# Kernel optimization log

Hardware: AMD Instinct MI355X
Metric: run time of the kernel (lower is better)

Reference implementation:

```python
import jax, jax.numpy as jnp
import numpy as np

B, N, NEV, E, D, L = 4, 20000, 100000, 400000, 64, 3

def setup_inputs() -> dict:
    key = jax.random.key(0)
    ks = jax.random.split(key, 12)
    x = jax.random.normal(ks[0], (B, N, 3), dtype=jnp.float32)
    # channel 0 is the susceptible boolean mask (0/1)
    mask0 = (jax.random.uniform(ks[1], (B, N)) < 0.3).astype(jnp.float32)
    x = x.at[..., 0].set(mask0)
    dag_edge_index = jax.random.randint(ks[2], (2, E), 0, NEV, dtype=jnp.int64)
    event_to_node = jax.random.randint(ks[3], (NEV,), 0, N, dtype=jnp.int64)
    event_src_node = jax.random.randint(ks[4], (NEV,), 0, N, dtype=jnp.int64)
    s = 1.0 / np.sqrt(D)
    Wp = jax.random.normal(ks[5], (6, D), dtype=jnp.float32) * (1.0 / np.sqrt(6))
    bp = jnp.zeros((D,), dtype=jnp.float32)
    Ws = jax.random.normal(ks[6], (L, D, D), dtype=jnp.float32) * s
    Wa = jax.random.normal(ks[7], (L, D, D), dtype=jnp.float32) * s
    ba = jnp.zeros((L, D), dtype=jnp.float32)
    Wo = jax.random.normal(ks[8], (D,), dtype=jnp.float32) * s
    bo = jnp.zeros((), dtype=jnp.float32)
    return {"x": x, "Wp": Wp, "bp": bp, "Ws": Ws, "Wa": Wa, "ba": ba,
            "Wo": Wo, "bo": bo, "dag_edge_index": dag_edge_index,
            "event_to_node": event_to_node, "event_src_node": event_src_node}

def reference(x, Wp, bp, Ws, Wa, ba, Wo, bo, dag_edge_index, event_to_node, event_src_node):
    n_events = event_src_node.shape[0]
    # event features: [B, n_events, 6] -> project -> ReLU
    ev_feat = jnp.concatenate([x[:, event_src_node, :], x[:, event_to_node, :]], axis=-1)
    h = jax.nn.relu(ev_feat @ Wp + bp)  # [B, n_events, D]
    # reversed DAG edges: src = dag[1], dst = dag[0]
    src_e, dst_e = dag_edge_index[1], dag_edge_index[0]
    deg = jnp.zeros((n_events,), h.dtype).at[dst_e].add(1.0)
    deg = jnp.maximum(deg, 1.0)[None, :, None]
    for l in range(Ws.shape[0]):
        agg = jnp.zeros_like(h).at[:, dst_e].add(h[:, src_e])  # scatter-add mean agg
        h = jax.nn.relu(h @ Ws[l] + (agg / deg) @ Wa[l] + ba[l])
    # aggregate events back to nodes (mean)
    node_emb = jnp.zeros((x.shape[0], x.shape[1], h.shape[-1]), h.dtype).at[:, event_to_node].add(h)
    count = jnp.zeros((x.shape[1],), h.dtype).at[event_to_node].add(1.0)
    node_emb = node_emb / jnp.maximum(count, 1.0)[None, :, None]
    scores = node_emb @ Wo + bo  # [B, N]
    susceptible = x[..., 0] > 0
    scores = jnp.where(susceptible, -jnp.inf, scores)
    return jax.nn.log_softmax(scores, axis=-1)
```

## Files before the change

### kernel.cpp

```cpp
#include <hip/hip_runtime.h>
#include <hip/hip_bf16.h>
#include <math.h>

constexpr int B   = 4;
constexpr int N   = 20000;
constexpr int NEV = 100000;
constexpr int E   = 400000;
constexpr int D   = 64;
constexpr int L   = 3;
constexpr int CAP = 32;
constexpr int CHUNK = 625;
constexpr size_t HBYTES = (size_t)B * NEV * D + 256;

typedef short  short8 __attribute__((ext_vector_type(8)));
typedef float  f32x4  __attribute__((ext_vector_type(4)));
typedef float  f32x2  __attribute__((ext_vector_type(2)));


__device__ inline unsigned short f2bu(float f) {
  union { __hip_bfloat16 b; unsigned short s; } u;
  u.b = __float2bfloat16(f);
  return u.s;
}
__device__ inline unsigned packbf(float lo, float hi) {
  return ((unsigned)f2bu(hi) << 16) | (unsigned)f2bu(lo);
}
__device__ inline void cvt16(float* a, uint4 v) {
  unsigned vv[4] = {v.x, v.y, v.z, v.w};
#pragma unroll
  for (int i = 0; i < 4; ++i) {
    f32x2 lo = __builtin_amdgcn_cvt_pk_f32_fp8((int)vv[i], false);
    f32x2 hi = __builtin_amdgcn_cvt_pk_f32_fp8((int)vv[i], true);
    a[4 * i + 0] = lo[0]; a[4 * i + 1] = lo[1];
    a[4 * i + 2] = hi[0]; a[4 * i + 3] = hi[1];
  }
}
__device__ inline void add16(float* a, uint4 v) {
  unsigned vv[4] = {v.x, v.y, v.z, v.w};
#pragma unroll
  for (int i = 0; i < 4; ++i) {
    f32x2 lo = __builtin_amdgcn_cvt_pk_f32_fp8((int)vv[i], false);
    f32x2 hi = __builtin_amdgcn_cvt_pk_f32_fp8((int)vv[i], true);
    a[4 * i + 0] += lo[0]; a[4 * i + 1] += lo[1];
    a[4 * i + 2] += hi[0]; a[4 * i + 3] += hi[1];
  }
}
__device__ inline short8 pack8(const float* f) {
  union { unsigned u[4]; short8 s; } r;
#pragma unroll
  for (int i = 0; i < 4; ++i) r.u[i] = packbf(f[2 * i], f[2 * i + 1]);
  return r.s;
}
__device__ __forceinline__ void round4(const unsigned char* gb,
                                       const int* cr, int p, float* a) {
  int4 idx = *(const int4*)(cr + p);
  uint4 v0 = *(const uint4*)(gb + (size_t)idx.x * 256);
  uint4 v1 = *(const uint4*)(gb + (size_t)idx.y * 256);
  uint4 v2 = *(const uint4*)(gb + (size_t)idx.z * 256);
  uint4 v3 = *(const uint4*)(gb + (size_t)idx.w * 256);
  add16(a, v0); add16(a, v1); add16(a, v2); add16(a, v3);
}


__global__ void k_zero(float4* __restrict__ p, int n4) {
  int i = blockIdx.x * blockDim.x + threadIdx.x;
  if (i < n4) p[i] = make_float4(0.f, 0.f, 0.f, 0.f);
}

__global__ void k_fill(int4* __restrict__ csrc4,
                       uint4* __restrict__ h0z, uint4* __restrict__ h1z) {
  int i = blockIdx.x * blockDim.x + threadIdx.x;
  if (i < NEV * CAP / 4) csrc4[i] = make_int4(NEV, NEV, NEV, NEV);
  int z = i - NEV * CAP / 4;
  if (z >= 0 && z < 16) h0z[z] = make_uint4(0u, 0u, 0u, 0u);
  if (z >= 16 && z < 32) h1z[z - 16] = make_uint4(0u, 0u, 0u, 0u);
}

__global__ void k_prep(const int* __restrict__ dag,
                       int* __restrict__ cnt,
                       int* __restrict__ csrc,
                       const int* __restrict__ e2n,
                       int* __restrict__ ncount,
                       const float* __restrict__ Ws,
                       const float* __restrict__ Wa,
                       unsigned short* __restrict__ Wt) {
  int bid = blockIdx.x;
  if (bid < 1563) {
    int i = bid * 256 + threadIdx.x;
    if (i < E) {
      int dst = dag[i];
      int src = dag[E + i];
      int pos = atomicAdd(&cnt[dst], 1);
      if (pos < CAP) csrc[dst * CAP + pos] = src;
    }
  } else if (bid < 1954) {
    int i = (bid - 1563) * 256 + threadIdx.x;
    if (i < NEV) atomicAdd(&ncount[e2n[i]], 1);
  } else {
    int i = (bid - 1954) * 256 + threadIdx.x;
    int l  = i >> 13;
    int r  = i & 8191;
    int n  = r >> 7;
    int s2 = r & 127;
    int hf = s2 >> 6, s = s2 & 63;
    int b  = ((s >> 3) & 3) * 16 + (s >> 5) * 8 + (s & 7);
    int c  = (b & 3) * 16 + (b >> 2);
    float v = hf ? Wa[l * 4096 + c * 64 + n]
                 : Ws[l * 4096 + c * 64 + n];
    Wt[l * 8192 + n * 128 + s2] = f2bu(v);
  }
}

__global__ __launch_bounds__(256) void k_proj(const float* __restrict__ x,
                                              const float* __restrict__ Wp,
                                              const float* __restrict__ bp,
                                              const int* __restrict__ esrc,
                                              const int* __restrict__ e2n,
                                              unsigned* __restrict__ h,
                                              float* __restrict__ nscore) {
  int gid = blockIdx.x * blockDim.x + threadIdx.x;
  if (gid < B * N) nscore[gid] = 0.f;
  const int lane = threadIdx.x & 63;
  const int e    = gid >> 6;
  int sn = esrc[e], tn = e2n[e];
  float xval = 0.f;
  if (lane < 24) {
    int bl = lane / 6, rem = lane % 6;
    int node = (rem < 3) ? sn : tn;
    xval = x[(size_t)(bl * N + node) * 3 + (rem < 3 ? rem : rem - 3)];
  }
  const int b = lane >> 4, p = lane & 15;
  float xv[6];
#pragma unroll
  for (int k = 0; k < 6; ++k) xv[k] = __shfl(xval, b * 6 + k, 64);
  float a[4];
#pragma unroll
  for (int t = 0; t < 4; ++t) {
    int d = p + 16 * t;
    float acc = bp[d];
#pragma unroll
    for (int k = 0; k < 6; ++k) acc += xv[k] * Wp[k * 64 + d];
    a[t] = fmaxf(acc, 0.f);
  }
  int w = __builtin_amdgcn_cvt_pk_fp8_f32(a[0], a[1], 0, false);
  w     = __builtin_amdgcn_cvt_pk_fp8_f32(a[2], a[3], w, true);
  h[e * 64 + lane] = (unsigned)w;
}

template <bool LAST>
__global__ __launch_bounds__(256, 4) void k_layer(
    const unsigned short* __restrict__ Wt,
    const float* __restrict__ ba,
    const float* __restrict__ Wo,
    const int* __restrict__ e2n,
    const int* __restrict__ cnt,
    const int* __restrict__ csrc,
    const unsigned char* __restrict__ h_in,
    unsigned char* __restrict__ h_out,
    float* __restrict__ nscore) {
  const int tid  = threadIdx.x;
  const int wv   = tid >> 6, lane = tid & 63;
  const int e0   = blockIdx.x * 32;
  const int r0   = e0 * 4;
  const int m    = lane & 15, q = lane >> 4;
  const int el   = m >> 2;
  const int bb   = m & 3;
  const int eA   = e0 + wv * 4 + el;
  const int eB   = e0 + 16 + wv * 4 + el;

  const int* crA = csrc + (size_t)eA * CAP;
  const int* crB = csrc + (size_t)eB * CAP;
  int4 iA = *(const int4*)crA;
  int4 iB = *(const int4*)crB;
  uint4 vdA = *(const uint4*)(h_in + (size_t)(r0 + wv * 16 + m) * 64 + q * 16);
  uint4 vdB = *(const uint4*)(h_in + (size_t)(r0 + 64 + wv * 16 + m) * 64 + q * 16);
  int cA = cnt[eA];
  int cB = cnt[eB];

  const unsigned char* gb = h_in + bb * 64 + q * 16;
  float aA[16], aB[16];
#pragma unroll
  for (int i = 0; i < 16; ++i) { aA[i] = 0.f; aB[i] = 0.f; }
  {
    uint4 vA0 = *(const uint4*)(gb + (size_t)iA.x * 256);
    uint4 vA1 = *(const uint4*)(gb + (size_t)iA.y * 256);
    uint4 vA2 = *(const uint4*)(gb + (size_t)iA.z * 256);
    uint4 vA3 = *(const uint4*)(gb + (size_t)iA.w * 256);
    uint4 vB0 = *(const uint4*)(gb + (size_t)iB.x * 256);
    uint4 vB1 = *(const uint4*)(gb + (size_t)iB.y * 256);
    uint4 vB2 = *(const uint4*)(gb + (size_t)iB.z * 256);
    uint4 vB3 = *(const uint4*)(gb + (size_t)iB.w * 256);
    add16(aA, vA0); add16(aA, vA1); add16(aA, vA2); add16(aA, vA3);
    add16(aB, vB0); add16(aB, vB1); add16(aB, vB2); add16(aB, vB3);
  }
  int ccA = min(cA, CAP), ccA16 = min(ccA, 16);
  int ccB = min(cB, CAP), ccB16 = min(ccB, 16);
  for (int p = 4; p < ccA16; p += 4) round4(gb, crA, p, aA);
  for (int p = 4; p < ccB16; p += 4) round4(gb, crB, p, aB);
  for (int j = 16; j < ccA; ++j)
    add16(aA, *(const uint4*)(gb + (size_t)crA[j] * 256));
  for (int j = 16; j < ccB; ++j)
    add16(aB, *(const uint4*)(gb + (size_t)crB[j] * 256));
  {
    float invA = 1.f / fmaxf((float)cA, 1.f);
    float invB = 1.f / fmaxf((float)cB, 1.f);
#pragma unroll
    for (int i = 0; i < 16; ++i) { aA[i] *= invA; aB[i] *= invB; }
  }
  short8 agA0 = pack8(aA), agA1 = pack8(aA + 8);
  short8 agB0 = pack8(aB), agB1 = pack8(aB + 8);

  short8 adA0, adA1, adB0, adB1;
  {
    float f[16];
    cvt16(f, vdA); adA0 = pack8(f); adA1 = pack8(f + 8);
    cvt16(f, vdB); adB0 = pack8(f); adB1 = pack8(f + 8);
  }

  f32x4 accA[4], accB[4];
#pragma unroll
  for (int t = 0; t < 4; ++t) {
    float bv = ba[t * 16 + m];
    accA[t] = (f32x4){bv, bv, bv, bv};
    accB[t] = accA[t];
  }
  const unsigned short* wb = Wt + m * 128 + q * 8;
#pragma unroll
  for (int t = 0; t < 4; ++t) {
    short8 b0 = *(const short8*)(wb + t * 2048 + 0);
    short8 b1 = *(const short8*)(wb + t * 2048 + 32);
    short8 b2 = *(const short8*)(wb + t * 2048 + 64);
    short8 b3 = *(const short8*)(wb + t * 2048 + 96);
    accA[t] = __builtin_amdgcn_mfma_f32_16x16x32_bf16(adA0, b0, accA[t], 0, 0, 0);
    accA[t] = __builtin_amdgcn_mfma_f32_16x16x32_bf16(adA1, b1, accA[t], 0, 0, 0);
    accA[t] = __builtin_amdgcn_mfma_f32_16x16x32_bf16(agA0, b2, accA[t], 0, 0, 0);
    accA[t] = __builtin_amdgcn_mfma_f32_16x16x32_bf16(agA1, b3, accA[t], 0, 0, 0);
    accB[t] = __builtin_amdgcn_mfma_f32_16x16x32_bf16(adB0, b0, accB[t], 0, 0, 0);
    accB[t] = __builtin_amdgcn_mfma_f32_16x16x32_bf16(adB1, b1, accB[t], 0, 0, 0);
    accB[t] = __builtin_amdgcn_mfma_f32_16x16x32_bf16(agB0, b2, accB[t], 0, 0, 0);
    accB[t] = __builtin_amdgcn_mfma_f32_16x16x32_bf16(agB1, b3, accB[t], 0, 0, 0);
  }

  if constexpr (!LAST) {
#pragma unroll
    for (int g = 0; g < 2; ++g) {
      const f32x4* ac = g ? accB : accA;
#pragma unroll
      for (int r = 0; r < 4; ++r) {
        int w = __builtin_amdgcn_cvt_pk_fp8_f32(fmaxf(ac[0][r], 0.f),
                                                fmaxf(ac[1][r], 0.f), 0, false);
        w     = __builtin_amdgcn_cvt_pk_fp8_f32(fmaxf(ac[2][r], 0.f),
                                                fmaxf(ac[3][r], 0.f), w, true);
        int grow = r0 + g * 64 + wv * 16 + q * 4 + r;
        ((unsigned*)h_out)[grow * 16 + m] = (unsigned)w;
      }
    }
  } else {
    float w0 = Wo[m], w1 = Wo[16 + m], w2 = Wo[32 + m], w3 = Wo[48 + m];
#pragma unroll
    for (int g = 0; g < 2; ++g) {
      const f32x4* ac = g ? accB : accA;
#pragma unroll
      for (int r = 0; r < 4; ++r) {
        float v = fmaxf(ac[0][r], 0.f) * w0 + fmaxf(ac[1][r], 0.f) * w1
                + fmaxf(ac[2][r], 0.f) * w2 + fmaxf(ac[3][r], 0.f) * w3;
        v += __shfl_xor(v, 1, 64);
        v += __shfl_xor(v, 2, 64);
        v += __shfl_xor(v, 4, 64);
        v += __shfl_xor(v, 8, 64);
        if (m == 0) {
          int grow = r0 + g * 64 + wv * 16 + q * 4 + r;
          int e = grow >> 2, b = grow & 3;
          atomicAdd(&nscore[b * N + e2n[e]], v);
        }
      }
    }
  }
}

__device__ inline float ls_score(const float* nscore, const int* ncount,
                                 const float* x, float bov, int b, int n) {
  return (x[(size_t)(b * N + n) * 3] > 0.f)
             ? -INFINITY
             : nscore[b * N + n] / fmaxf((float)ncount[n], 1.f) + bov;
}

__global__ __launch_bounds__(256) void k_ls1(const float* __restrict__ nscore,
                                             const int* __restrict__ ncount,
                                             const float* __restrict__ x,
                                             const float* __restrict__ bo,
                                             float* __restrict__ pmax,
                                             float* __restrict__ psum,
                                             float* __restrict__ sc) {
  const int b = blockIdx.x >> 5, ch = blockIdx.x & 31;
  const int n0 = ch * CHUNK;
  const int tid = threadIdx.x;
  const float bov = bo[0];
  float s0 = -INFINITY, s1 = -INFINITY, s2 = -INFINITY;
  if (tid < CHUNK) {
    s0 = ls_score(nscore, ncount, x, bov, b, n0 + tid);
    sc[b * N + n0 + tid] = s0;
  }
  if (tid + 256 < CHUNK) {
    s1 = ls_score(nscore, ncount, x, bov, b, n0 + tid + 256);
    sc[b * N + n0 + tid + 256] = s1;
  }
  if (tid + 512 < CHUNK) {
    s2 = ls_score(nscore, ncount, x, bov, b, n0 + tid + 512);
    sc[b * N + n0 + tid + 512] = s2;
  }
  float m = fmaxf(fmaxf(s0, s1), s2);
  __shared__ float red[4];
#pragma unroll
  for (int o = 32; o; o >>= 1) m = fmaxf(m, __shfl_xor(m, o, 64));
  if ((tid & 63) == 0) red[tid >> 6] = m;
  __syncthreads();
  float pm = fmaxf(fmaxf(red[0], red[1]), fmaxf(red[2], red[3]));
  float pm2 = (pm == -INFINITY) ? 0.f : pm;
  float e = expf(s0 - pm2) + expf(s1 - pm2) + expf(s2 - pm2);
#pragma unroll
  for (int o = 32; o; o >>= 1) e += __shfl_xor(e, o, 64);
  __syncthreads();
  if ((tid & 63) == 0) red[tid >> 6] = e;
  __syncthreads();
  if (tid == 0) {
    pmax[blockIdx.x] = pm;
    psum[blockIdx.x] = red[0] + red[1] + red[2] + red[3];
  }
}

__global__ __launch_bounds__(256) void k_ls3(const float* __restrict__ pmax,
                                             const float* __restrict__ psum,
                                             const float* __restrict__ sc,
                                             float* __restrict__ out) {
  const int b = blockIdx.x >> 5, ch = blockIdx.x & 31;
  const int n0 = ch * CHUNK;
  const int tid = threadIdx.x;
  __shared__ float sgm, slse;
  if (tid < 64) {
    float pm = (tid < 32) ? pmax[b * 32 + tid] : -INFINITY;
    float ps = (tid < 32) ? psum[b * 32 + tid] : 0.f;
    float gm = pm;
#pragma unroll
    for (int o = 32; o; o >>= 1) gm = fmaxf(gm, __shfl_xor(gm, o, 64));
    float gm2 = (gm == -INFINITY) ? 0.f : gm;
    float c = (pm == -INFINITY) ? 0.f : ps * expf(pm - gm2);
#pragma unroll
    for (int o = 32; o; o >>= 1) c += __shfl_xor(c, o, 64);
    if (tid == 0) { sgm = gm; slse = logf(c); }
  }
  __syncthreads();
  const float gm = sgm, lse = slse;
  for (int i = tid; i < CHUNK; i += 256) {
    int n = n0 + i;
    out[b * N + n] = fmaxf(sc[b * N + n] - gm - lse, -3.0e38f);
  }
}

extern "C" void kernel_launch(void* const* d_in, const int* in_sizes, int n_in,
                              void* d_out, int out_size, void* d_ws, size_t ws_size,
                              hipStream_t stream) {
  const float* x   = (const float*)d_in[0];
  const float* Wp  = (const float*)d_in[1];
  const float* bp  = (const float*)d_in[2];
  const float* Ws  = (const float*)d_in[3];
  const float* Wa  = (const float*)d_in[4];
  const float* ba  = (const float*)d_in[5];
  const float* Wo  = (const float*)d_in[6];
  const float* bo  = (const float*)d_in[7];
  const int*   dag = (const int*)d_in[8];
  const int*   e2n = (const int*)d_in[9];
  const int*   esr = (const int*)d_in[10];

  int*   ws     = (int*)d_ws;
  int*   cnt    = ws;
  int*   ncount = ws + 100000;
  float* nscore = (float*)(ws + 120000);
  float* pmax   = (float*)(ws + 200000);
  float* psum   = (float*)(ws + 200128);
  int*   csrc   = ws + 200704;
  unsigned short* Wt = (unsigned short*)(ws + 3400704);
  unsigned char* h0 = (unsigned char*)(ws + 3406912);
  unsigned char* h1 = h0 + HBYTES;
  float* sc     = (float*)(h1 + HBYTES);
  float* out    = (float*)d_out;

  k_zero<<<(30000 + 255) / 256, 256, 0, stream>>>((float4*)ws, 30000);
  k_fill<<<(NEV * CAP / 4 + 32 + 255) / 256, 256, 0, stream>>>(
      (int4*)csrc, (uint4*)(h0 + (size_t)NEV * 256), (uint4*)(h1 + (size_t)NEV * 256));
  k_prep<<<2050, 256, 0, stream>>>(dag, cnt, csrc, e2n, ncount, Ws, Wa, Wt);
  k_proj<<<(B * NEV * 16) / 256, 256, 0, stream>>>(x, Wp, bp, esr, e2n,
                                                   (unsigned*)h0, nscore);

  k_layer<false><<<NEV / 32, 256, 0, stream>>>(Wt,         ba,       Wo, e2n,
                                               cnt, csrc, h0, h1, nscore);
  k_layer<false><<<NEV / 32, 256, 0, stream>>>(Wt + 8192,  ba + D,   Wo, e2n,
                                               cnt, csrc, h1, h0, nscore);
  k_layer<true><<<NEV / 32, 256, 0, stream>>>(Wt + 16384,  ba + 2*D, Wo, e2n,
                                              cnt, csrc, h0, h1, nscore);

  k_ls1<<<B * 32, 256, 0, stream>>>(nscore, ncount, x, bo, pmax, psum, sc);
  k_ls3<<<B * 32, 256, 0, stream>>>(pmax, psum, sc, out);
}
```

Baseline: 295.1 us.

## Split neighbor list into 8-slot head and overflow tail, gather 8 unconditionally

The padded 32-slot CSR neighbor table becomes a dense 8-entry head array plus a 24-entry overflow array. Each layer now issues 8 unconditional neighbor gathers per event up front, since mean in-degree is about 4, and loops over the tail only when needed. The fill kernel now initialises only the small head array. Accumulators move to packed float2 vectors so the compiler can use packed adds. The aim is less fill traffic, smaller index loads and more memory-level parallelism, at the cost of wasted gathers of the zero padding row for low-degree events and more registers.

```diff
diff --git a/kernel.cpp b/kernel.cpp
--- a/kernel.cpp
+++ b/kernel.cpp
@@ -25,40 +25,29 @@
 __device__ inline unsigned packbf(float lo, float hi) {
   return ((unsigned)f2bu(hi) << 16) | (unsigned)f2bu(lo);
 }
-__device__ inline void cvt16(float* a, uint4 v) {
+__device__ __forceinline__ void add16p(f32x2* a2, uint4 v) {
   unsigned vv[4] = {v.x, v.y, v.z, v.w};
 #pragma unroll
   for (int i = 0; i < 4; ++i) {
     f32x2 lo = __builtin_amdgcn_cvt_pk_f32_fp8((int)vv[i], false);
     f32x2 hi = __builtin_amdgcn_cvt_pk_f32_fp8((int)vv[i], true);
-    a[4 * i + 0] = lo[0]; a[4 * i + 1] = lo[1];
-    a[4 * i + 2] = hi[0]; a[4 * i + 3] = hi[1];
-  }
-}
-__device__ inline void add16(float* a, uint4 v) {
+    a2[2 * i]     += lo;
+    a2[2 * i + 1] += hi;
+  }
+}
+__device__ __forceinline__ void cvt16p(f32x2* a2, uint4 v) {
   unsigned vv[4] = {v.x, v.y, v.z, v.w};
 #pragma unroll
   for (int i = 0; i < 4; ++i) {
-    f32x2 lo = __builtin_amdgcn_cvt_pk_f32_fp8((int)vv[i], false);
-    f32x2 hi = __builtin_amdgcn_cvt_pk_f32_fp8((int)vv[i], true);
-    a[4 * i + 0] += lo[0]; a[4 * i + 1] += lo[1];
-    a[4 * i + 2] += hi[0]; a[4 * i + 3] += hi[1];
-  }
-}
-__device__ inline short8 pack8(const float* f) {
+    a2[2 * i]     = __builtin_amdgcn_cvt_pk_f32_fp8((int)vv[i], false);
+    a2[2 * i + 1] = __builtin_amdgcn_cvt_pk_f32_fp8((int)vv[i], true);
+  }
+}
+__device__ __forceinline__ short8 pack8p(const f32x2* f) {
   union { unsigned u[4]; short8 s; } r;
 #pragma unroll
-  for (int i = 0; i < 4; ++i) r.u[i] = packbf(f[2 * i], f[2 * i + 1]);
+  for (int i = 0; i < 4; ++i) r.u[i] = packbf(f[i][0], f[i][1]);
   return r.s;
-}
-__device__ __forceinline__ void round4(const unsigned char* gb,
-                                       const int* cr, int p, float* a) {
-  int4 idx = *(const int4*)(cr + p);
-  uint4 v0 = *(const uint4*)(gb + (size_t)idx.x * 256);
-  uint4 v1 = *(const uint4*)(gb + (size_t)idx.y * 256);
-  uint4 v2 = *(const uint4*)(gb + (size_t)idx.z * 256);
-  uint4 v3 = *(const uint4*)(gb + (size_t)idx.w * 256);
-  add16(a, v0); add16(a, v1); add16(a, v2); add16(a, v3);
 }
 
 
@@ -67,18 +56,19 @@
   if (i < n4) p[i] = make_float4(0.f, 0.f, 0.f, 0.f);
 }
 
-__global__ void k_fill(int4* __restrict__ csrc4,
+__global__ void k_fill(int4* __restrict__ lo4,
                        uint4* __restrict__ h0z, uint4* __restrict__ h1z) {
   int i = blockIdx.x * blockDim.x + threadIdx.x;
-  if (i < NEV * CAP / 4) csrc4[i] = make_int4(NEV, NEV, NEV, NEV);
-  int z = i - NEV * CAP / 4;
+  if (i < NEV * 8 / 4) lo4[i] = make_int4(NEV, NEV, NEV, NEV);
+  int z = i - NEV * 8 / 4;
   if (z >= 0 && z < 16) h0z[z] = make_uint4(0u, 0u, 0u, 0u);
   if (z >= 16 && z < 32) h1z[z - 16] = make_uint4(0u, 0u, 0u, 0u);
 }
 
 __global__ void k_prep(const int* __restrict__ dag,
                        int* __restrict__ cnt,
-                       int* __restrict__ csrc,
+                       int* __restrict__ csrc_lo,
+                       int* __restrict__ csrc_hi,
                        const int* __restrict__ e2n,
                        int* __restrict__ ncount,
                        const float* __restrict__ Ws,
@@ -91,7 +81,8 @@
       int dst = dag[i];
       int src = dag[E + i];
       int pos = atomicAdd(&cnt[dst], 1);
-      if (pos < CAP) csrc[dst * CAP + pos] = src;
+      if (pos < 8)        csrc_lo[dst * 8 + pos] = src;
+      else if (pos < CAP) csrc_hi[dst * 24 + (pos - 8)] = src;
     }
   } else if (bid < 1954) {
     int i = (bid - 1563) * 256 + threadIdx.x;
@@ -154,7 +145,8 @@
     const float* __restrict__ Wo,
     const int* __restrict__ e2n,
     const int* __restrict__ cnt,
-    const int* __restrict__ csrc,
+    const int* __restrict__ csrc_lo,
+    const int* __restrict__ csrc_hi,
     const unsigned char* __restrict__ h_in,
     unsigned char* __restrict__ h_out,
     float* __restrict__ nscore) {
@@ -168,53 +160,68 @@
   const int eA   = e0 + wv * 4 + el;
   const int eB   = e0 + 16 + wv * 4 + el;
 
-  const int* crA = csrc + (size_t)eA * CAP;
-  const int* crB = csrc + (size_t)eB * CAP;
-  int4 iA = *(const int4*)crA;
-  int4 iB = *(const int4*)crB;
+  const int* clA = csrc_lo + (size_t)eA * 8;
+  const int* clB = csrc_lo + (size_t)eB * 8;
+  int4 iA0 = *(const int4*)clA;
+  int4 iA1 = *(const int4*)(clA + 4);
+  int4 iB0 = *(const int4*)clB;
+  int4 iB1 = *(const int4*)(clB + 4);
   uint4 vdA = *(const uint4*)(h_in + (size_t)(r0 + wv * 16 + m) * 64 + q * 16);
   uint4 vdB = *(const uint4*)(h_in + (size_t)(r0 + 64 + wv * 16 + m) * 64 + q * 16);
   int cA = cnt[eA];
   int cB = cnt[eB];
 
   const unsigned char* gb = h_in + bb * 64 + q * 16;
-  float aA[16], aB[16];
-#pragma unroll
-  for (int i = 0; i < 16; ++i) { aA[i] = 0.f; aB[i] = 0.f; }
+  f32x2 aA[8], aB[8];
+#pragma unroll
+  for (int i = 0; i < 8; ++i) { aA[i] = (f32x2){0.f, 0.f}; aB[i] = (f32x2){0.f, 0.f}; }
   {
-    uint4 vA0 = *(const uint4*)(gb + (size_t)iA.x * 256);
-    uint4 vA1 = *(const uint4*)(gb + (size_t)iA.y * 256);
-    uint4 vA2 = *(const uint4*)(gb + (size_t)iA.z * 256);
-    uint4 vA3 = *(const uint4*)(gb + (size_t)iA.w * 256);
-    uint4 vB0 = *(const uint4*)(gb + (size_t)iB.x * 256);
-    uint4 vB1 = *(const uint4*)(gb + (size_t)iB.y * 256);
-    uint4 vB2 = *(const uint4*)(gb + (size_t)iB.z * 256);
-    uint4 vB3 = *(const uint4*)(gb + (size_t)iB.w * 256);
-    add16(aA, vA0); add16(aA, vA1); add16(aA, vA2); add16(aA, vA3);
-    add16(aB, vB0); add16(aB, vB1); add16(aB, vB2); add16(aB, vB3);
-  }
-  int ccA = min(cA, CAP), ccA16 = min(ccA, 16);
-  int ccB = min(cB, CAP), ccB16 = min(ccB, 16);
-  for (int p = 4; p < ccA16; p += 4) round4(gb, crA, p, aA);
-  for (int p = 4; p < ccB16; p += 4) round4(gb, crB, p, aB);
-  for (int j = 16; j < ccA; ++j)
-    add16(aA, *(const uint4*)(gb + (size_t)crA[j] * 256));
-  for (int j = 16; j < ccB; ++j)
-    add16(aB, *(const uint4*)(gb + (size_t)crB[j] * 256));
+    uint4 gA0 = *(const uint4*)(gb + (size_t)iA0.x * 256);
+    uint4 gA1 = *(const uint4*)(gb + (size_t)iA0.y * 256);
+    uint4 gA2 = *(const uint4*)(gb + (size_t)iA0.z * 256);
+    uint4 gA3 = *(const uint4*)(gb + (size_t)iA0.w * 256);
+    uint4 gA4 = *(const uint4*)(gb + (size_t)iA1.x * 256);
+    uint4 gA5 = *(const uint4*)(gb + (size_t)iA1.y * 256);
+    uint4 gA6 = *(const uint4*)(gb + (size_t)iA1.z * 256);
+    uint4 gA7 = *(const uint4*)(gb + (size_t)iA1.w * 256);
+    uint4 gB0 = *(const uint4*)(gb + (size_t)iB0.x * 256);
+    uint4 gB1 = *(const uint4*)(gb + (size_t)iB0.y * 256);
+    uint4 gB2 = *(const uint4*)(gb + (size_t)iB0.z * 256);
+    uint4 gB3 = *(const uint4*)(gb + (size_t)iB0.w * 256);
+    uint4 gB4 = *(const uint4*)(gb + (size_t)iB1.x * 256);
+    uint4 gB5 = *(const uint4*)(gb + (size_t)iB1.y * 256);
+    uint4 gB6 = *(const uint4*)(gb + (size_t)iB1.z * 256);
+    uint4 gB7 = *(const uint4*)(gb + (size_t)iB1.w * 256);
+    add16p(aA, gA0); add16p(aA, gA1); add16p(aA, gA2); add16p(aA, gA3);
+    add16p(aA, gA4); add16p(aA, gA5); add16p(aA, gA6); add16p(aA, gA7);
+    add16p(aB, gB0); add16p(aB, gB1); add16p(aB, gB2); add16p(aB, gB3);
+    add16p(aB, gB4); add16p(aB, gB5); add16p(aB, gB6); add16p(aB, gB7);
+  }
+  int ccA = min(cA, CAP), ccB = min(cB, CAP);
+  if (ccA > 8) {
+    const int* chA = csrc_hi + (size_t)eA * 24;
+    for (int j = 8; j < ccA; ++j)
+      add16p(aA, *(const uint4*)(gb + (size_t)chA[j - 8] * 256));
+  }
+  if (ccB > 8) {
+    const int* chB = csrc_hi + (size_t)eB * 24;
+    for (int j = 8; j < ccB; ++j)
+      add16p(aB, *(const uint4*)(gb + (size_t)chB[j - 8] * 256));
+  }
   {
     float invA = 1.f / fmaxf((float)cA, 1.f);
     float invB = 1.f / fmaxf((float)cB, 1.f);
 #pragma unroll
-    for (int i = 0; i < 16; ++i) { aA[i] *= invA; aB[i] *= invB; }
-  }
-  short8 agA0 = pack8(aA), agA1 = pack8(aA + 8);
-  short8 agB0 = pack8(aB), agB1 = pack8(aB + 8);
+    for (int i = 0; i < 8; ++i) { aA[i] = aA[i] * invA; aB[i] = aB[i] * invB; }
+  }
+  short8 agA0 = pack8p(aA), agA1 = pack8p(aA + 4);
+  short8 agB0 = pack8p(aB), agB1 = pack8p(aB + 4);
 
   short8 adA0, adA1, adB0, adB1;
   {
-    float f[16];
-    cvt16(f, vdA); adA0 = pack8(f); adA1 = pack8(f + 8);
-    cvt16(f, vdB); adB0 = pack8(f); adB1 = pack8(f + 8);
+    f32x2 f[8];
+    cvt16p(f, vdA); adA0 = pack8p(f); adA1 = pack8p(f + 4);
+    cvt16p(f, vdB); adB0 = pack8p(f); adB1 = pack8p(f + 4);
   }
 
   f32x4 accA[4], accB[4];
@@ -378,7 +385,8 @@
   float* nscore = (float*)(ws + 120000);
   float* pmax   = (float*)(ws + 200000);
   float* psum   = (float*)(ws + 200128);
-  int*   csrc   = ws + 200704;
+  int*   csrc_lo = ws + 200704;
+  int*   csrc_hi = ws + 1000704;
   unsigned short* Wt = (unsigned short*)(ws + 3400704);
   unsigned char* h0 = (unsigned char*)(ws + 3406912);
   unsigned char* h1 = h0 + HBYTES;
@@ -386,18 +394,19 @@
   float* out    = (float*)d_out;
 
   k_zero<<<(30000 + 255) / 256, 256, 0, stream>>>((float4*)ws, 30000);
-  k_fill<<<(NEV * CAP / 4 + 32 + 255) / 256, 256, 0, stream>>>(
-      (int4*)csrc, (uint4*)(h0 + (size_t)NEV * 256), (uint4*)(h1 + (size_t)NEV * 256));
-  k_prep<<<2050, 256, 0, stream>>>(dag, cnt, csrc, e2n, ncount, Ws, Wa, Wt);
+  k_fill<<<(NEV * 2 + 32 + 255) / 256, 256, 0, stream>>>(
+      (int4*)csrc_lo, (uint4*)(h0 + (size_t)NEV * 256), (uint4*)(h1 + (size_t)NEV * 256));
+  k_prep<<<2050, 256, 0, stream>>>(dag, cnt, csrc_lo, csrc_hi, e2n, ncount,
+                                   Ws, Wa, Wt);
   k_proj<<<(B * NEV * 16) / 256, 256, 0, stream>>>(x, Wp, bp, esr, e2n,
                                                    (unsigned*)h0, nscore);
 
   k_layer<false><<<NEV / 32, 256, 0, stream>>>(Wt,         ba,       Wo, e2n,
-                                               cnt, csrc, h0, h1, nscore);
+                                               cnt, csrc_lo, csrc_hi, h0, h1, nscore);
   k_layer<false><<<NEV / 32, 256, 0, stream>>>(Wt + 8192,  ba + D,   Wo, e2n,
-                                               cnt, csrc, h1, h0, nscore);
+                                               cnt, csrc_lo, csrc_hi, h1, h0, nscore);
   k_layer<true><<<NEV / 32, 256, 0, stream>>>(Wt + 16384,  ba + 2*D, Wo, e2n,
-                                              cnt, csrc, h0, h1, nscore);
+                                              cnt, csrc_lo, csrc_hi, h0, h1, nscore);
 
   k_ls1<<<B * 32, 256, 0, stream>>>(nscore, ncount, x, bo, pmax, psum, sc);
   k_ls3<<<B * 32, 256, 0, stream>>>(pmax, psum, sc, out);
```

Measured after the change: 409.6 us. 38.8% more time.
